# Kernel tuning notes

Measured on AMD Instinct MI355X. Metric: run time of the kernel, lower is better.

## Reference

```python
import jax, jax.numpy as jnp
import numpy as np

A_DIM = 6
VBR = jnp.array([300.0, 750.0, 1200.0, 1850.0, 2850.0, 4300.0])
MAX_BR = 4300.0
BUF = 30000.0  # buffer_size fixed to 30000 each forward
N_STEPS = 6    # unrolled iterations in the source (cooked_bw[0]..cooked_bw[5])


def _conv_feat(x, w, b):
    # 1-channel valid Conv1d(kernel=4) + ReLU, flattened channel-major like torch .view
    L = x.shape[0]
    idx = jnp.arange(L - 3)[:, None] + jnp.arange(4)[None, :]
    win = x[idx]                                   # (L-3, 4)
    out = jax.nn.relu(win @ w[:, 0, :].T + b)      # (L-3, 128)
    return out.T.reshape(-1)                       # (128*(L-3),)


def setup_inputs() -> dict:
    key = jax.random.key(0)
    ks = jax.random.split(key, 12)
    s = 0.1
    return {
        "inp": jax.random.uniform(ks[0], (8, 8), jnp.float32) + 0.1,
        "conv_w": jax.random.normal(ks[1], (128, 1, 4), jnp.float32) * s,
        "conv_b": jax.random.normal(ks[2], (128,), jnp.float32) * s,
        "w0": jax.random.normal(ks[3], (128, 1), jnp.float32) * s,
        "b0": jax.random.normal(ks[4], (128,), jnp.float32) * s,
        "w1": jax.random.normal(ks[5], (128, 1), jnp.float32) * s,
        "b1": jax.random.normal(ks[6], (128,), jnp.float32) * s,
        "w2": jax.random.normal(ks[7], (128, 1), jnp.float32) * s,
        "b2": jax.random.normal(ks[8], (128,), jnp.float32) * s,
        "w3": jax.random.normal(ks[9], (128, 2048), jnp.float32) * 0.02,
        "b3": jax.random.normal(ks[10], (128,), jnp.float32) * s,
        "w4": jax.random.normal(ks[11], (6, 128), jnp.float32) * s,
        "b4": jnp.zeros((6,), jnp.float32),
    }


def reference(inp, conv_w, conv_b, w0, b0, w1, b1, w2, b2, w3, b3, w4, b4):
    state = inp[:6, :]          # (6, 8)
    bw = inp[6, :]              # cooked bandwidth trace
    vs = inp[7, 0]              # base video chunk size
    vcs = vs * jnp.array([1.0, 2.0, 4.0, 8.0, 16.0, 32.0])  # video_chunk_sizes

    def net(st):
        s0 = jax.nn.relu(st[0, -1] * w0[:, 0] + b0)
        s1 = jax.nn.relu(st[1, -1] * w1[:, 0] + b1)
        s2 = _conv_feat(st[2, :], conv_w, conv_b)          # 640
        s3 = _conv_feat(st[3, :], conv_w, conv_b)          # 640
        s4 = _conv_feat(st[4, :A_DIM], conv_w, conv_b)     # 384
        s5 = st[4, -1] * w2[:, 0] + b2                     # no relu (matches source)
        feat = jnp.concatenate([s0, s1, s2, s3, s4, s5])   # (2048,)
        h = jax.nn.relu(w3 @ feat + b3)
        return w4 @ h + b4                                 # (6,)

    for i in range(N_STEPS):
        logits = net(state)
        a = jnp.argmax(logits)
        state = jnp.roll(state, -1, axis=1)
        delay = vcs[a] / bw[i] - BUF
        state = state.at[0, -1].set(VBR[a] / MAX_BR)
        state = state.at[1, -1].set(BUF / 1000.0 / 10.0)
        state = state.at[2, -1].set(vcs[a] / delay / 1000.0)
        state = state.at[3, -1].set(delay / 1000.0 / 10.0)
        state = state.at[4, :A_DIM].set(vcs / 1e6)
        state = state.at[5, -1].set((7.0 - i) / 8.0)

    return net(state)
```

## Files before the change

### kernel.cpp

```cpp
#include <hip/hip_runtime.h>

#define NBLK 32
#define TPB  256
#define FSTRIDE 32
#define PSTRIDE 64

__device__ __forceinline__ float relu_(float x) { return fmaxf(x, 0.f); }


__launch_bounds__(TPB, 1)
__global__ void actor_kernel(
    const float* __restrict__ inp,
    const float* __restrict__ conv_w, const float* __restrict__ conv_b,
    const float* __restrict__ w0, const float* __restrict__ b0,
    const float* __restrict__ w1, const float* __restrict__ b1,
    const float* __restrict__ w2, const float* __restrict__ b2,
    const float* __restrict__ w3, const float* __restrict__ b3,
    const float* __restrict__ w4, const float* __restrict__ b4,
    float* __restrict__ out, int* __restrict__ flags,
    float* __restrict__ partials)
{
    const int tid = threadIdx.x;
    const int b   = blockIdx.x;

    __shared__ __align__(16) float lw3[4 * 2048];
    __shared__ __align__(16) float lfeat[2048];
    __shared__ __align__(16) float lc2[512], lc3[512];
    __shared__ float lbase2[128], lbase3[128], ls5[128];
    __shared__ float ls0[6 * 128];
    __shared__ float ltmp[512];
    __shared__ __align__(16) float lcw[512];
    __shared__ float lcb[128];
    __shared__ float lw0v[128], lb0v[128], lw1v[128], lb1v[128];
    __shared__ float lw2v[128], lb2v[128], lb3v[128];
    __shared__ float lw4[768], lb4v[8];
    __shared__ float st2[8], st3[8], st4[8];
    __shared__ float sx[8];
    __shared__ float lbw[8];
    __shared__ float h_lds[4], hv_lds[4 * 8];
    __shared__ float red[48];

    {
        const float4* g4 = (const float4*)(w3 + b * 4 * 2048);
        float4* l4 = (float4*)lw3;
        for (int idx = tid; idx < 2048; idx += TPB) l4[idx] = g4[idx];
    }
    for (int idx = tid; idx < 512; idx += TPB) lcw[idx] = conv_w[idx];
    if (tid < 128) {
        lcb[tid]  = conv_b[tid];
        lw0v[tid] = w0[tid]; lb0v[tid] = b0[tid];
        lw1v[tid] = w1[tid]; lb1v[tid] = b1[tid];
        lw2v[tid] = w2[tid]; lb2v[tid] = b2[tid];
        lb3v[tid] = b3[tid];
    }
    for (int idx = tid; idx < 768; idx += TPB) lw4[idx] = w4[idx];
    if (tid < 6) lb4v[tid] = b4[tid];
    if (tid < 8) {
        st2[tid] = inp[16 + tid];
        st3[tid] = inp[24 + tid];
        st4[tid] = inp[32 + tid];
        lbw[tid] = inp[48 + tid];
    }
    if (tid == 0) {
        sx[0] = inp[7];   sx[1] = inp[15];
        sx[2] = inp[39];  sx[3] = inp[32];
        sx[4] = inp[56];
    }
    __syncthreads();

    if (tid < 128) {
        const float vb[6] = {300.f, 750.f, 1200.f, 1850.f, 2850.f, 4300.f};
        #pragma unroll
        for (int v = 0; v < 6; ++v)
            ls0[v * 128 + tid] = relu_(vb[v] * (1.f / 4300.f) * lw0v[tid] + lb0v[tid]);
        ltmp[tid] = relu_(3.0f * lw1v[tid] + lb1v[tid]);
    }
    for (int m = tid; m < 384; m += TPB) {
        int c = m / 3, w = m - c * 3;
        float a = lcb[c];
        #pragma unroll
        for (int k = 0; k < 4; ++k)
            a += sx[4] * (float)(1 << (w + k)) * 1e-6f * lcw[c * 4 + k];
        ltmp[128 + m] = relu_(a);
    }
    __syncthreads();

    const int wv = tid >> 6, lane = tid & 63;
    const float* wr = lw3 + wv * 2048;
    const float bias3 = lb3v[b * 4 + wv];

    float hs0p[6], hs14p;
    #pragma unroll
    for (int v = 0; v < 6; ++v)
        hs0p[v] = wr[lane] * ls0[v * 128 + lane] + wr[64 + lane] * ls0[v * 128 + 64 + lane];
    hs14p = wr[128 + lane] * ltmp[lane] + wr[192 + lane] * ltmp[64 + lane];
    #pragma unroll
    for (int k = 0; k < 6; ++k) {
        int m = lane + 64 * k;
        hs14p += wr[1536 + m] * ltmp[128 + m];
    }

    const float VBRc[6] = {300.f, 750.f, 1200.f, 1850.f, 2850.f, 4300.f};

    for (int g = 0; g < 3; ++g) {
        const int i = 2 * g;

        if (tid < 128) {
            lfeat[tid]        = relu_(sx[0] * lw0v[tid] + lb0v[tid]);
            lfeat[1920 + tid] =        sx[2] * lw2v[tid] + lb2v[tid];
            lbase2[tid] = st2[5] * lcw[tid*4] + st2[6] * lcw[tid*4+1]
                        + st2[7] * lcw[tid*4+2] + lcb[tid];
            lbase3[tid] = st3[5] * lcw[tid*4] + st3[6] * lcw[tid*4+1]
                        + st3[7] * lcw[tid*4+2] + lcb[tid];
            ls5[tid] = sx[3] * lw2v[tid] + lb2v[tid];
        } else {
            int j = tid - 128;
            lfeat[128 + j] = relu_(sx[1] * lw1v[j] + lb1v[j]);
        }
        for (int m = tid; m < 640; m += TPB) {
            int c = m / 5, w = m - c * 5;
            float a2 = lcb[c], a3 = lcb[c];
            #pragma unroll
            for (int k = 0; k < 4; ++k) {
                float cw = lcw[c * 4 + k];
                a2 += st2[w + k] * cw;
                a3 += st3[w + k] * cw;
            }
            lfeat[256 + m] = relu_(a2);
            lfeat[896 + m] = relu_(a3);
        }
        for (int m = tid; m < 384; m += TPB) {
            int c = m / 3, w = m - c * 3;
            float a4 = lcb[c];
            #pragma unroll
            for (int k = 0; k < 4; ++k) a4 += st4[w + k] * lcw[c * 4 + k];
            lfeat[1536 + m] = relu_(a4);
        }
        for (int m = tid; m < 512; m += TPB) {
            int c = m >> 2, w = m & 3;
            float a2 = lcb[c], a3 = lcb[c];
            #pragma unroll
            for (int k = 0; k < 4; ++k) {
                float cw = lcw[c * 4 + k];
                a2 += st2[w + 1 + k] * cw;
                a3 += st3[w + 1 + k] * cw;
            }
            lc2[m] = relu_(a2);
            lc3[m] = relu_(a3);
        }
        __syncthreads();

        float acc_i;
        {
            const float4* w4p = (const float4*)wr;
            const float4* f4p = (const float4*)lfeat;
            float4 acc = make_float4(0.f, 0.f, 0.f, 0.f);
            #pragma unroll
            for (int it = 0; it < 8; ++it) {
                float4 a = w4p[it * 64 + lane];
                float4 f = f4p[it * 64 + lane];
                acc.x += a.x * f.x; acc.y += a.y * f.y;
                acc.z += a.z * f.z; acc.w += a.w * f.w;
            }
            acc_i = (acc.x + acc.y) + (acc.z + acc.w);
        }

        float acc_c = hs14p
                    + wr[1920 + lane] * ls5[lane]
                    + wr[1984 + lane] * ls5[64 + lane];
        #pragma unroll
        for (int k = 0; k < 8; ++k) {
            int m = lane + 64 * k;
            int col = 256 + (m >> 2) * 5 + (m & 3);
            acc_c += wr[col] * lc2[m] + wr[640 + col] * lc3[m];
        }

        float n2[6], n3[6];
        {
            float bwi = lbw[i], vs = sx[4];
            #pragma unroll
            for (int v = 0; v < 6; ++v) {
                float vca   = vs * (float)(1 << v);
                float delay = vca / bwi - 30000.f;
                n2[v] = vca / delay * 1e-3f;
                n3[v] = delay * 1e-4f;
            }
        }
        float accv[6];
        #pragma unroll
        for (int v = 0; v < 6; ++v) accv[v] = hs0p[v];
        #pragma unroll
        for (int t = 0; t < 2; ++t) {
            int c = lane + 64 * t;
            float cw3 = lcw[c * 4 + 3];
            float bb2 = lbase2[c], bb3 = lbase3[c];
            float wc2 = wr[256 + c * 5 + 4], wc3 = wr[896 + c * 5 + 4];
            #pragma unroll
            for (int v = 0; v < 6; ++v)
                accv[v] += relu_(bb2 + n2[v] * cw3) * wc2
                         + relu_(bb3 + n3[v] * cw3) * wc3;
        }

        #pragma unroll
        for (int off = 32; off > 0; off >>= 1) {
            acc_i += __shfl_xor(acc_i, off);
            acc_c += __shfl_xor(acc_c, off);
            #pragma unroll
            for (int v = 0; v < 6; ++v) accv[v] += __shfl_xor(accv[v], off);
        }
        if (lane == 0) {
            h_lds[wv] = relu_(acc_i + bias3);
            #pragma unroll
            for (int v = 0; v < 6; ++v)
                hv_lds[wv * 8 + v] = relu_(acc_c + accv[v] + bias3);
        }
        __syncthreads();

        if (tid < 42) {
            int q = tid / 6, t = tid - q * 6;
            float p = 0.f;
            if (q == 0) {
                #pragma unroll
                for (int w = 0; w < 4; ++w) p += lw4[t * 128 + b * 4 + w] * h_lds[w];
            } else {
                #pragma unroll
                for (int w = 0; w < 4; ++w) p += lw4[t * 128 + b * 4 + w] * hv_lds[w * 8 + (q - 1)];
            }
            __hip_atomic_store(&partials[(g * NBLK + b) * PSTRIDE + tid], p,
                               __ATOMIC_RELAXED, __HIP_MEMORY_SCOPE_AGENT);
        }
        __syncthreads();
        if (tid == 0)
            __hip_atomic_store(&flags[b * FSTRIDE], g + 1,
                               __ATOMIC_RELEASE, __HIP_MEMORY_SCOPE_AGENT);
        if (tid < NBLK) {
            while (__hip_atomic_load(&flags[tid * FSTRIDE], __ATOMIC_ACQUIRE,
                                     __HIP_MEMORY_SCOPE_AGENT) < g + 1)
                __builtin_amdgcn_s_sleep(1);
        }
        __syncthreads();

        if (tid < 42) {
            float p = lb4v[tid % 6];
            #pragma unroll
            for (int bb = 0; bb < NBLK; ++bb)
                p += __hip_atomic_load(&partials[(g * NBLK + bb) * PSTRIDE + tid],
                                       __ATOMIC_RELAXED, __HIP_MEMORY_SCOPE_AGENT);
            red[tid] = p;
        }
        __syncthreads();
        if (tid == 0) {
            float best = red[0]; int a0 = 0;
            #pragma unroll
            for (int r = 1; r < 6; ++r) if (red[r] > best) { best = red[r]; a0 = r; }
            best = red[6 + 6 * a0]; int a1 = 0;
            #pragma unroll
            for (int r = 1; r < 6; ++r)
                if (red[6 + 6 * a0 + r] > best) { best = red[6 + 6 * a0 + r]; a1 = r; }

            {
                float vca = sx[4] * (float)(1 << a0);
                float delay = vca / lbw[i] - 30000.f;
                sx[0] = VBRc[a0] * (1.f / 4300.f);
                sx[1] = 3.0f;
                #pragma unroll
                for (int c = 0; c < 7; ++c) { st2[c] = st2[c + 1]; st3[c] = st3[c + 1]; }
                st2[7] = vca / delay * 1e-3f;
                st3[7] = delay * 1e-4f;
                sx[2] = sx[3]; sx[3] = sx[4] * 1e-6f;
                #pragma unroll
                for (int j = 0; j < 6; ++j) st4[j] = sx[4] * (float)(1 << j) * 1e-6f;
            }
            {
                float vca = sx[4] * (float)(1 << a1);
                float delay = vca / lbw[i + 1] - 30000.f;
                sx[0] = VBRc[a1] * (1.f / 4300.f);
                sx[1] = 3.0f;
                #pragma unroll
                for (int c = 0; c < 7; ++c) { st2[c] = st2[c + 1]; st3[c] = st3[c + 1]; }
                st2[7] = vca / delay * 1e-3f;
                st3[7] = delay * 1e-4f;
                sx[2] = sx[3]; sx[3] = sx[4] * 1e-6f;
                #pragma unroll
                for (int j = 0; j < 6; ++j) st4[j] = sx[4] * (float)(1 << j) * 1e-6f;
            }
        }
        __syncthreads();
    }

    if (tid < 128) {
        lfeat[tid]        = relu_(sx[0] * lw0v[tid] + lb0v[tid]);
        lfeat[1920 + tid] =        sx[2] * lw2v[tid] + lb2v[tid];
    } else {
        int j = tid - 128;
        lfeat[128 + j] = relu_(sx[1] * lw1v[j] + lb1v[j]);
    }
    for (int m = tid; m < 640; m += TPB) {
        int c = m / 5, w = m - c * 5;
        float a2 = lcb[c], a3 = lcb[c];
        #pragma unroll
        for (int k = 0; k < 4; ++k) {
            float cw = lcw[c * 4 + k];
            a2 += st2[w + k] * cw;
            a3 += st3[w + k] * cw;
        }
        lfeat[256 + m] = relu_(a2);
        lfeat[896 + m] = relu_(a3);
    }
    for (int m = tid; m < 384; m += TPB) {
        int c = m / 3, w = m - c * 3;
        float a4 = lcb[c];
        #pragma unroll
        for (int k = 0; k < 4; ++k) a4 += st4[w + k] * lcw[c * 4 + k];
        lfeat[1536 + m] = relu_(a4);
    }
    __syncthreads();
    {
        const float4* w4p = (const float4*)wr;
        const float4* f4p = (const float4*)lfeat;
        float4 acc = make_float4(0.f, 0.f, 0.f, 0.f);
        #pragma unroll
        for (int it = 0; it < 8; ++it) {
            float4 a = w4p[it * 64 + lane];
            float4 f = f4p[it * 64 + lane];
            acc.x += a.x * f.x; acc.y += a.y * f.y;
            acc.z += a.z * f.z; acc.w += a.w * f.w;
        }
        float s = (acc.x + acc.y) + (acc.z + acc.w);
        #pragma unroll
        for (int off = 32; off > 0; off >>= 1) s += __shfl_xor(s, off);
        if (lane == 0) h_lds[wv] = relu_(s + bias3);
    }
    __syncthreads();
    if (tid < 6) {
        float p = 0.f;
        #pragma unroll
        for (int w = 0; w < 4; ++w) p += lw4[tid * 128 + b * 4 + w] * h_lds[w];
        __hip_atomic_store(&partials[(3 * NBLK + b) * PSTRIDE + tid], p,
                           __ATOMIC_RELAXED, __HIP_MEMORY_SCOPE_AGENT);
    }
    __syncthreads();
    if (tid == 0)
        __hip_atomic_store(&flags[b * FSTRIDE], 4,
                           __ATOMIC_RELEASE, __HIP_MEMORY_SCOPE_AGENT);
    if (b == 0) {
        if (tid < NBLK) {
            while (__hip_atomic_load(&flags[tid * FSTRIDE], __ATOMIC_ACQUIRE,
                                     __HIP_MEMORY_SCOPE_AGENT) < 4)
                __builtin_amdgcn_s_sleep(1);
        }
        __syncthreads();
        if (tid < 6) {
            float p = lb4v[tid];
            #pragma unroll
            for (int bb = 0; bb < NBLK; ++bb)
                p += __hip_atomic_load(&partials[(3 * NBLK + bb) * PSTRIDE + tid],
                                       __ATOMIC_RELAXED, __HIP_MEMORY_SCOPE_AGENT);
            out[tid] = p;
        }
    }
}

extern "C" void kernel_launch(void* const* d_in, const int* in_sizes, int n_in,
                              void* d_out, int out_size, void* d_ws, size_t ws_size,
                              hipStream_t stream) {
    const float* inp    = (const float*)d_in[0];
    const float* conv_w = (const float*)d_in[1];
    const float* conv_b = (const float*)d_in[2];
    const float* w0     = (const float*)d_in[3];
    const float* b0     = (const float*)d_in[4];
    const float* w1     = (const float*)d_in[5];
    const float* b1     = (const float*)d_in[6];
    const float* w2     = (const float*)d_in[7];
    const float* b2     = (const float*)d_in[8];
    const float* w3     = (const float*)d_in[9];
    const float* b3     = (const float*)d_in[10];
    const float* w4     = (const float*)d_in[11];
    const float* b4     = (const float*)d_in[12];

    int*   flags    = (int*)d_ws;
    float* partials = (float*)((char*)d_ws + 8192);

    actor_kernel<<<NBLK, TPB, 0, stream>>>(inp, conv_w, conv_b,
                                           w0, b0, w1, b1, w2, b2,
                                           w3, b3, w4, b4,
                                           (float*)d_out, flags, partials);
}
```

Measured before the change: 99.95 us.

## Pack partials with epoch tags into 64-bit words to drop flag barrier

Each block now publishes every partial logit as a 64-bit word holding the float value and the step tag. This replaces the separate partial store plus release flag and block barrier. Readers poll the tagged words directly, with the gather split across 168 threads and then reduced in shared memory. The goal is to remove the extra syncthreads, the flag round-trip and the serial 32-way load per thread on the inter-block exchange path. In exchange it polls many more addresses, and any stale tags left in the workspace from earlier launches could match early.

```diff
diff --git a/kernel.cpp b/kernel.cpp
--- a/kernel.cpp
+++ b/kernel.cpp
@@ -2,8 +2,6 @@
 
 #define NBLK 32
 #define TPB  256
-#define FSTRIDE 32
-#define PSTRIDE 64
 
 __device__ __forceinline__ float relu_(float x) { return fmaxf(x, 0.f); }
 
@@ -17,8 +15,7 @@
     const float* __restrict__ w2, const float* __restrict__ b2,
     const float* __restrict__ w3, const float* __restrict__ b3,
     const float* __restrict__ w4, const float* __restrict__ b4,
-    float* __restrict__ out, int* __restrict__ flags,
-    float* __restrict__ partials)
+    float* __restrict__ out, unsigned long long* __restrict__ pub)
 {
     const int tid = threadIdx.x;
     const int b   = blockIdx.x;
@@ -38,6 +35,7 @@
     __shared__ float sx[8];
     __shared__ float lbw[8];
     __shared__ float h_lds[4], hv_lds[4 * 8];
+    __shared__ float s_red[192];
     __shared__ float red[48];
 
     {
@@ -226,29 +224,46 @@
                 #pragma unroll
                 for (int w = 0; w < 4; ++w) p += lw4[t * 128 + b * 4 + w] * hv_lds[w * 8 + (q - 1)];
             }
-            __hip_atomic_store(&partials[(g * NBLK + b) * PSTRIDE + tid], p,
+            unsigned long long val =
+                ((unsigned long long)__float_as_uint(p) << 32) | (unsigned)(g + 1);
+            __hip_atomic_store(&pub[(g * NBLK + b) * 64 + tid], val,
                                __ATOMIC_RELAXED, __HIP_MEMORY_SCOPE_AGENT);
         }
-        __syncthreads();
-        if (tid == 0)
-            __hip_atomic_store(&flags[b * FSTRIDE], g + 1,
-                               __ATOMIC_RELEASE, __HIP_MEMORY_SCOPE_AGENT);
-        if (tid < NBLK) {
-            while (__hip_atomic_load(&flags[tid * FSTRIDE], __ATOMIC_ACQUIRE,
-                                     __HIP_MEMORY_SCOPE_AGENT) < g + 1)
+
+        if (tid < 168) {
+            int j = tid >> 2, part = tid & 3;
+            const unsigned long long* base = &pub[(g * NBLK + part * 8) * 64 + j];
+            unsigned long long v[8];
+            #pragma unroll
+            for (int k = 0; k < 8; ++k)
+                v[k] = __hip_atomic_load(base + k * 64, __ATOMIC_ACQUIRE,
+                                         __HIP_MEMORY_SCOPE_AGENT);
+            for (;;) {
+                bool all = true;
+                #pragma unroll
+                for (int k = 0; k < 8; ++k)
+                    all = all && ((unsigned)v[k] == (unsigned)(g + 1));
+                if (all) break;
                 __builtin_amdgcn_s_sleep(1);
-        }
-        __syncthreads();
-
-        if (tid < 42) {
-            float p = lb4v[tid % 6];
-            #pragma unroll
-            for (int bb = 0; bb < NBLK; ++bb)
-                p += __hip_atomic_load(&partials[(g * NBLK + bb) * PSTRIDE + tid],
-                                       __ATOMIC_RELAXED, __HIP_MEMORY_SCOPE_AGENT);
-            red[tid] = p;
-        }
-        __syncthreads();
+                #pragma unroll
+                for (int k = 0; k < 8; ++k)
+                    if ((unsigned)v[k] != (unsigned)(g + 1))
+                        v[k] = __hip_atomic_load(base + k * 64, __ATOMIC_ACQUIRE,
+                                                 __HIP_MEMORY_SCOPE_AGENT);
+            }
+            float p = 0.f;
+            #pragma unroll
+            for (int k = 0; k < 8; ++k)
+                p += __uint_as_float((unsigned)(v[k] >> 32));
+            s_red[j * 4 + part] = p;
+        }
+        __syncthreads();
+        if (tid < 42)
+            red[tid] = lb4v[tid % 6]
+                     + ((s_red[tid * 4] + s_red[tid * 4 + 1])
+                      + (s_red[tid * 4 + 2] + s_red[tid * 4 + 3]));
+        __syncthreads();
+
         if (tid == 0) {
             float best = red[0]; int a0 = 0;
             #pragma unroll
@@ -336,26 +351,29 @@
         float p = 0.f;
         #pragma unroll
         for (int w = 0; w < 4; ++w) p += lw4[tid * 128 + b * 4 + w] * h_lds[w];
-        __hip_atomic_store(&partials[(3 * NBLK + b) * PSTRIDE + tid], p,
+        unsigned long long val =
+            ((unsigned long long)__float_as_uint(p) << 32) | 4u;
+        __hip_atomic_store(&pub[(3 * NBLK + b) * 64 + tid], val,
                            __ATOMIC_RELAXED, __HIP_MEMORY_SCOPE_AGENT);
     }
-    __syncthreads();
-    if (tid == 0)
-        __hip_atomic_store(&flags[b * FSTRIDE], 4,
-                           __ATOMIC_RELEASE, __HIP_MEMORY_SCOPE_AGENT);
     if (b == 0) {
-        if (tid < NBLK) {
-            while (__hip_atomic_load(&flags[tid * FSTRIDE], __ATOMIC_ACQUIRE,
-                                     __HIP_MEMORY_SCOPE_AGENT) < 4)
+        if (tid < 192) {
+            int j = tid >> 5, bb = tid & 31;
+            unsigned long long v =
+                __hip_atomic_load(&pub[(3 * NBLK + bb) * 64 + j],
+                                  __ATOMIC_ACQUIRE, __HIP_MEMORY_SCOPE_AGENT);
+            while ((unsigned)v != 4u) {
                 __builtin_amdgcn_s_sleep(1);
+                v = __hip_atomic_load(&pub[(3 * NBLK + bb) * 64 + j],
+                                      __ATOMIC_ACQUIRE, __HIP_MEMORY_SCOPE_AGENT);
+            }
+            s_red[j * 32 + bb] = __uint_as_float((unsigned)(v >> 32));
         }
         __syncthreads();
         if (tid < 6) {
             float p = lb4v[tid];
             #pragma unroll
-            for (int bb = 0; bb < NBLK; ++bb)
-                p += __hip_atomic_load(&partials[(3 * NBLK + bb) * PSTRIDE + tid],
-                                       __ATOMIC_RELAXED, __HIP_MEMORY_SCOPE_AGENT);
+            for (int bb = 0; bb < NBLK; ++bb) p += s_red[tid * 32 + bb];
             out[tid] = p;
         }
     }
@@ -378,11 +396,10 @@
     const float* w4     = (const float*)d_in[11];
     const float* b4     = (const float*)d_in[12];
 
-    int*   flags    = (int*)d_ws;
-    float* partials = (float*)((char*)d_ws + 8192);
+    unsigned long long* pub = (unsigned long long*)d_ws;
 
     actor_kernel<<<NBLK, TPB, 0, stream>>>(inp, conv_w, conv_b,
                                            w0, b0, w1, b1, w2, b2,
                                            w3, b3, w4, b4,
-                                           (float*)d_out, flags, partials);
+                                           (float*)d_out, pub);
 }
```

New measurement: 113.7 us. +13.7%, slower.

## Speculatively evaluate final two steps for all 36 action pairs to cut a grid barrier

Applied to the files above, without the earlier changes.

Replaces the last loop iteration and the final network pass with one phase. For step 4, each block computes logits for all six step-5 candidates and for all 36 (a4, a5) action pairs of the final pass. Block 0 reduces the 258 partials, picks the actions by argmax and outputs the matching logits. This removes one cross-block flag round-trip, but adds much more per-thread work and register use (42 extra accumulators) and a larger partials buffer.

```diff
diff --git a/kernel.cpp b/kernel.cpp
--- a/kernel.cpp
+++ b/kernel.cpp
@@ -3,7 +3,7 @@
 #define NBLK 32
 #define TPB  256
 #define FSTRIDE 32
-#define PSTRIDE 64
+#define PSTRIDE 320
 
 __device__ __forceinline__ float relu_(float x) { return fmaxf(x, 0.f); }
 
@@ -38,7 +38,10 @@
     __shared__ float sx[8];
     __shared__ float lbw[8];
     __shared__ float h_lds[4], hv_lds[4 * 8];
+    __shared__ float hf_lds[4 * 40];
     __shared__ float red[48];
+    __shared__ float red2[264];
+    __shared__ int   ssel;
 
     {
         const float4* g4 = (const float4*)(w3 + b * 4 * 2048);
@@ -102,7 +105,7 @@
 
     const float VBRc[6] = {300.f, 750.f, 1200.f, 1850.f, 2850.f, 4300.f};
 
-    for (int g = 0; g < 3; ++g) {
+    for (int g = 0; g < 2; ++g) {
         const int i = 2 * g;
 
         if (tid < 128) {
@@ -288,75 +291,212 @@
         __syncthreads();
     }
 
-    if (tid < 128) {
-        lfeat[tid]        = relu_(sx[0] * lw0v[tid] + lb0v[tid]);
-        lfeat[1920 + tid] =        sx[2] * lw2v[tid] + lb2v[tid];
-    } else {
-        int j = tid - 128;
-        lfeat[128 + j] = relu_(sx[1] * lw1v[j] + lb1v[j]);
-    }
-    for (int m = tid; m < 640; m += TPB) {
-        int c = m / 5, w = m - c * 5;
-        float a2 = lcb[c], a3 = lcb[c];
-        #pragma unroll
-        for (int k = 0; k < 4; ++k) {
-            float cw = lcw[c * 4 + k];
-            a2 += st2[w + k] * cw;
-            a3 += st3[w + k] * cw;
-        }
-        lfeat[256 + m] = relu_(a2);
-        lfeat[896 + m] = relu_(a3);
-    }
-    for (int m = tid; m < 384; m += TPB) {
-        int c = m / 3, w = m - c * 3;
-        float a4 = lcb[c];
-        #pragma unroll
-        for (int k = 0; k < 4; ++k) a4 += st4[w + k] * lcw[c * 4 + k];
-        lfeat[1536 + m] = relu_(a4);
-    }
-    __syncthreads();
     {
-        const float4* w4p = (const float4*)wr;
-        const float4* f4p = (const float4*)lfeat;
-        float4 acc = make_float4(0.f, 0.f, 0.f, 0.f);
-        #pragma unroll
-        for (int it = 0; it < 8; ++it) {
-            float4 a = w4p[it * 64 + lane];
-            float4 f = f4p[it * 64 + lane];
-            acc.x += a.x * f.x; acc.y += a.y * f.y;
-            acc.z += a.z * f.z; acc.w += a.w * f.w;
-        }
-        float s = (acc.x + acc.y) + (acc.z + acc.w);
-        #pragma unroll
-        for (int off = 32; off > 0; off >>= 1) s += __shfl_xor(s, off);
-        if (lane == 0) h_lds[wv] = relu_(s + bias3);
-    }
-    __syncthreads();
-    if (tid < 6) {
-        float p = 0.f;
-        #pragma unroll
-        for (int w = 0; w < 4; ++w) p += lw4[tid * 128 + b * 4 + w] * h_lds[w];
-        __hip_atomic_store(&partials[(3 * NBLK + b) * PSTRIDE + tid], p,
-                           __ATOMIC_RELAXED, __HIP_MEMORY_SCOPE_AGENT);
-    }
-    __syncthreads();
-    if (tid == 0)
-        __hip_atomic_store(&flags[b * FSTRIDE], 4,
-                           __ATOMIC_RELEASE, __HIP_MEMORY_SCOPE_AGENT);
-    if (b == 0) {
-        if (tid < NBLK) {
-            while (__hip_atomic_load(&flags[tid * FSTRIDE], __ATOMIC_ACQUIRE,
-                                     __HIP_MEMORY_SCOPE_AGENT) < 4)
-                __builtin_amdgcn_s_sleep(1);
-        }
-        __syncthreads();
-        if (tid < 6) {
-            float p = lb4v[tid];
-            #pragma unroll
-            for (int bb = 0; bb < NBLK; ++bb)
-                p += __hip_atomic_load(&partials[(3 * NBLK + bb) * PSTRIDE + tid],
-                                       __ATOMIC_RELAXED, __HIP_MEMORY_SCOPE_AGENT);
-            out[tid] = p;
+        const int i = 4;
+
+        if (tid < 128) {
+            lfeat[tid]        = relu_(sx[0] * lw0v[tid] + lb0v[tid]);
+            lfeat[1920 + tid] =        sx[2] * lw2v[tid] + lb2v[tid];
+            lbase2[tid] = st2[5] * lcw[tid*4] + st2[6] * lcw[tid*4+1]
+                        + st2[7] * lcw[tid*4+2] + lcb[tid];
+            lbase3[tid] = st3[5] * lcw[tid*4] + st3[6] * lcw[tid*4+1]
+                        + st3[7] * lcw[tid*4+2] + lcb[tid];
+            ls5[tid] = sx[3] * lw2v[tid] + lb2v[tid];
+        } else {
+            int j = tid - 128;
+            lfeat[128 + j] = relu_(sx[1] * lw1v[j] + lb1v[j]);
+        }
+        for (int m = tid; m < 640; m += TPB) {
+            int c = m / 5, w = m - c * 5;
+            float a2 = lcb[c], a3 = lcb[c];
+            #pragma unroll
+            for (int k = 0; k < 4; ++k) {
+                float cw = lcw[c * 4 + k];
+                a2 += st2[w + k] * cw;
+                a3 += st3[w + k] * cw;
+            }
+            lfeat[256 + m] = relu_(a2);
+            lfeat[896 + m] = relu_(a3);
+        }
+        for (int m = tid; m < 384; m += TPB) {
+            int c = m / 3, w = m - c * 3;
+            float a4 = lcb[c];
+            #pragma unroll
+            for (int k = 0; k < 4; ++k) a4 += st4[w + k] * lcw[c * 4 + k];
+            lfeat[1536 + m] = relu_(a4);
+        }
+        for (int m = tid; m < 512; m += TPB) {
+            int c = m >> 2, w = m & 3;
+            float a2 = lcb[c], a3 = lcb[c];
+            #pragma unroll
+            for (int k = 0; k < 4; ++k) {
+                float cw = lcw[c * 4 + k];
+                a2 += st2[w + 1 + k] * cw;
+                a3 += st3[w + 1 + k] * cw;
+            }
+            lc2[m] = relu_(a2);
+            lc3[m] = relu_(a3);
+        }
+        __syncthreads();
+
+        float acc_i;
+        {
+            const float4* w4p = (const float4*)wr;
+            const float4* f4p = (const float4*)lfeat;
+            float4 acc = make_float4(0.f, 0.f, 0.f, 0.f);
+            #pragma unroll
+            for (int it = 0; it < 8; ++it) {
+                float4 a = w4p[it * 64 + lane];
+                float4 f = f4p[it * 64 + lane];
+                acc.x += a.x * f.x; acc.y += a.y * f.y;
+                acc.z += a.z * f.z; acc.w += a.w * f.w;
+            }
+            acc_i = (acc.x + acc.y) + (acc.z + acc.w);
+        }
+
+        float s5c = wr[1920 + lane] * ls5[lane] + wr[1984 + lane] * ls5[64 + lane];
+        float acc_c = hs14p + s5c;
+        #pragma unroll
+        for (int k = 0; k < 8; ++k) {
+            int m = lane + 64 * k;
+            int col = 256 + (m >> 2) * 5 + (m & 3);
+            acc_c += wr[col] * lc2[m] + wr[640 + col] * lc3[m];
+        }
+
+        float n24[6], n34[6], n25[6], n35[6];
+        {
+            float bw4 = lbw[4], bw5 = lbw[5], vs = sx[4];
+            #pragma unroll
+            for (int v = 0; v < 6; ++v) {
+                float vca = vs * (float)(1 << v);
+                float d4  = vca / bw4 - 30000.f;
+                float d5  = vca / bw5 - 30000.f;
+                n24[v] = vca / d4 * 1e-3f;  n34[v] = d4 * 1e-4f;
+                n25[v] = vca / d5 * 1e-3f;  n35[v] = d5 * 1e-4f;
+            }
+        }
+
+        float cw0a[2], cw1a[2], cw2a[2], cw3a[2], lb2a[2], lb3a[2];
+        float wc2a[2], wc3a[2], w3s2[2], w3s3[2], b42a[2], b43a[2];
+        float fcom = hs14p + s5c;
+        #pragma unroll
+        for (int t = 0; t < 2; ++t) {
+            int c = lane + 64 * t;
+            cw0a[t] = lcw[c*4];   cw1a[t] = lcw[c*4+1];
+            cw2a[t] = lcw[c*4+2]; cw3a[t] = lcw[c*4+3];
+            lb2a[t] = lbase2[c];  lb3a[t] = lbase3[c];
+            wc2a[t] = wr[256 + c*5 + 4]; wc3a[t] = wr[896 + c*5 + 4];
+            w3s2[t] = wr[256 + c*5 + 3]; w3s3[t] = wr[896 + c*5 + 3];
+            b42a[t] = st2[6]*cw0a[t] + st2[7]*cw1a[t] + lcb[c];
+            b43a[t] = st3[6]*cw0a[t] + st3[7]*cw1a[t] + lcb[c];
+            #pragma unroll
+            for (int w = 0; w < 3; ++w) {
+                float a2 = st2[2+w]*cw0a[t] + st2[3+w]*cw1a[t]
+                         + st2[4+w]*cw2a[t] + st2[5+w]*cw3a[t] + lcb[c];
+                float a3 = st3[2+w]*cw0a[t] + st3[3+w]*cw1a[t]
+                         + st3[4+w]*cw2a[t] + st3[5+w]*cw3a[t] + lcb[c];
+                fcom += relu_(a2) * wr[256 + c*5 + w] + relu_(a3) * wr[896 + c*5 + w];
+            }
+        }
+
+        float accv[6], accf[36];
+        #pragma unroll
+        for (int v4 = 0; v4 < 6; ++v4) {
+            float av = hs0p[v4];
+            float fv4 = fcom;
+            #pragma unroll
+            for (int t = 0; t < 2; ++t) {
+                float r2 = relu_(lb2a[t] + n24[v4] * cw3a[t]);
+                float r3 = relu_(lb3a[t] + n34[v4] * cw3a[t]);
+                av  += r2 * wc2a[t] + r3 * wc3a[t];
+                fv4 += r2 * w3s2[t] + r3 * w3s3[t];
+            }
+            accv[v4] = av;
+            #pragma unroll
+            for (int v5 = 0; v5 < 6; ++v5) {
+                float s = fv4 + hs0p[v5];
+                #pragma unroll
+                for (int t = 0; t < 2; ++t) {
+                    s += relu_(b42a[t] + n24[v4]*cw2a[t] + n25[v5]*cw3a[t]) * wc2a[t]
+                       + relu_(b43a[t] + n34[v4]*cw2a[t] + n35[v5]*cw3a[t]) * wc3a[t];
+                }
+                accf[v4 * 6 + v5] = s;
+            }
+        }
+
+        #pragma unroll
+        for (int off = 32; off > 0; off >>= 1) {
+            acc_i += __shfl_xor(acc_i, off);
+            acc_c += __shfl_xor(acc_c, off);
+            #pragma unroll
+            for (int v = 0; v < 6; ++v) accv[v] += __shfl_xor(accv[v], off);
+            #pragma unroll
+            for (int v = 0; v < 36; ++v) accf[v] += __shfl_xor(accf[v], off);
+        }
+        if (lane == 0) {
+            h_lds[wv] = relu_(acc_i + bias3);
+            #pragma unroll
+            for (int v = 0; v < 6; ++v)
+                hv_lds[wv * 8 + v] = relu_(acc_c + accv[v] + bias3);
+            #pragma unroll
+            for (int v = 0; v < 36; ++v)
+                hf_lds[wv * 40 + v] = relu_(accf[v] + bias3);
+        }
+        __syncthreads();
+
+        float* slot = &partials[(2 * NBLK + b) * PSTRIDE];
+        if (tid < 42) {
+            int q = tid / 6, t = tid - q * 6;
+            float p = 0.f;
+            if (q == 0) {
+                #pragma unroll
+                for (int w = 0; w < 4; ++w) p += lw4[t * 128 + b * 4 + w] * h_lds[w];
+            } else {
+                #pragma unroll
+                for (int w = 0; w < 4; ++w) p += lw4[t * 128 + b * 4 + w] * hv_lds[w * 8 + (q - 1)];
+            }
+            __hip_atomic_store(&slot[tid], p, __ATOMIC_RELAXED, __HIP_MEMORY_SCOPE_AGENT);
+        }
+        if (tid < 216) {
+            int combo = tid / 6, t = tid - combo * 6;
+            float p = 0.f;
+            #pragma unroll
+            for (int w = 0; w < 4; ++w) p += lw4[t * 128 + b * 4 + w] * hf_lds[w * 40 + combo];
+            __hip_atomic_store(&slot[42 + tid], p, __ATOMIC_RELAXED, __HIP_MEMORY_SCOPE_AGENT);
+        }
+        __syncthreads();
+        if (tid == 0)
+            __hip_atomic_store(&flags[b * FSTRIDE], 3,
+                               __ATOMIC_RELEASE, __HIP_MEMORY_SCOPE_AGENT);
+
+        if (b == 0) {
+            if (tid < NBLK) {
+                while (__hip_atomic_load(&flags[tid * FSTRIDE], __ATOMIC_ACQUIRE,
+                                         __HIP_MEMORY_SCOPE_AGENT) < 3)
+                    __builtin_amdgcn_s_sleep(1);
+            }
+            __syncthreads();
+            for (int v = tid; v < 258; v += TPB) {
+                float p = lb4v[v % 6];
+                #pragma unroll
+                for (int bb = 0; bb < NBLK; ++bb)
+                    p += __hip_atomic_load(&partials[(2 * NBLK + bb) * PSTRIDE + v],
+                                           __ATOMIC_RELAXED, __HIP_MEMORY_SCOPE_AGENT);
+                red2[v] = p;
+            }
+            __syncthreads();
+            if (tid == 0) {
+                float best = red2[0]; int a4 = 0;
+                #pragma unroll
+                for (int r = 1; r < 6; ++r) if (red2[r] > best) { best = red2[r]; a4 = r; }
+                best = red2[6 + 6 * a4]; int a5 = 0;
+                #pragma unroll
+                for (int r = 1; r < 6; ++r)
+                    if (red2[6 + 6 * a4 + r] > best) { best = red2[6 + 6 * a4 + r]; a5 = r; }
+                ssel = a4 * 6 + a5;
+            }
+            __syncthreads();
+            if (tid < 6) out[tid] = red2[42 + ssel * 6 + tid];
         }
     }
 }
```

New measurement: 102.2 us. +2.3%, slower.

## Precompute final-step features in registers and skip last state update pass

Applied to the files above, without the earlier changes.

During the last group, each lane precomputes the parts of the final network evaluation that do not depend on the last two chosen actions, keeping them in registers. The final forward pass then reduces to a few relu terms selected by the chosen actions, replacing the full feature rebuild, a barrier and the full 2048-wide dot product. Block 0's final reduction also loads the partials in parallel across threads into shared memory instead of issuing serial atomic loads from six threads. This adds register pressure and depends on the incremental decomposition staying exact for the rolled state.

```diff
diff --git a/kernel.cpp b/kernel.cpp
--- a/kernel.cpp
+++ b/kernel.cpp
@@ -39,6 +39,8 @@
     __shared__ float lbw[8];
     __shared__ float h_lds[4], hv_lds[4 * 8];
     __shared__ float red[48];
+    __shared__ float s_red[192];
+    __shared__ int   sact[2];
 
     {
         const float4* g4 = (const float4*)(w3 + b * 4 * 2048);
@@ -101,6 +103,10 @@
     }
 
     const float VBRc[6] = {300.f, 750.f, 1200.f, 1850.f, 2850.f, 4300.f};
+
+    float fcom_f = 0.f;
+    float lb2s[2], lb3s[2], b4f2[2], b4f3[2];
+    float cw2s[2], cw3s[2], w32s[2], w33s[2], w42s[2], w43s[2];
 
     for (int g = 0; g < 3; ++g) {
         const int i = 2 * g;
@@ -165,9 +171,8 @@
             acc_i = (acc.x + acc.y) + (acc.z + acc.w);
         }
 
-        float acc_c = hs14p
-                    + wr[1920 + lane] * ls5[lane]
-                    + wr[1984 + lane] * ls5[64 + lane];
+        float s5c = wr[1920 + lane] * ls5[lane] + wr[1984 + lane] * ls5[64 + lane];
+        float acc_c = hs14p + s5c;
         #pragma unroll
         for (int k = 0; k < 8; ++k) {
             int m = lane + 64 * k;
@@ -199,6 +204,27 @@
             for (int v = 0; v < 6; ++v)
                 accv[v] += relu_(bb2 + n2[v] * cw3) * wc2
                          + relu_(bb3 + n3[v] * cw3) * wc3;
+        }
+
+        if (g == 2) {
+            fcom_f = hs14p + s5c;
+            #pragma unroll
+            for (int t = 0; t < 2; ++t) {
+                int c = lane + 64 * t;
+                float c0 = lcw[c*4], c1 = lcw[c*4+1], c2 = lcw[c*4+2], c3 = lcw[c*4+3];
+                cw2s[t] = c2; cw3s[t] = c3;
+                lb2s[t] = lbase2[c];  lb3s[t] = lbase3[c];
+                b4f2[t] = st2[6]*c0 + st2[7]*c1 + lcb[c];
+                b4f3[t] = st3[6]*c0 + st3[7]*c1 + lcb[c];
+                w32s[t] = wr[256 + c*5 + 3]; w33s[t] = wr[896 + c*5 + 3];
+                w42s[t] = wr[256 + c*5 + 4]; w43s[t] = wr[896 + c*5 + 4];
+                #pragma unroll
+                for (int w = 0; w < 3; ++w) {
+                    float a2 = st2[2+w]*c0 + st2[3+w]*c1 + st2[4+w]*c2 + st2[5+w]*c3 + lcb[c];
+                    float a3 = st3[2+w]*c0 + st3[3+w]*c1 + st3[4+w]*c2 + st3[5+w]*c3 + lcb[c];
+                    fcom_f += relu_(a2) * wr[256 + c*5 + w] + relu_(a3) * wr[896 + c*5 + w];
+                }
+            }
         }
 
         #pragma unroll
@@ -258,78 +284,69 @@
             for (int r = 1; r < 6; ++r)
                 if (red[6 + 6 * a0 + r] > best) { best = red[6 + 6 * a0 + r]; a1 = r; }
 
-            {
-                float vca = sx[4] * (float)(1 << a0);
-                float delay = vca / lbw[i] - 30000.f;
-                sx[0] = VBRc[a0] * (1.f / 4300.f);
-                sx[1] = 3.0f;
-                #pragma unroll
-                for (int c = 0; c < 7; ++c) { st2[c] = st2[c + 1]; st3[c] = st3[c + 1]; }
-                st2[7] = vca / delay * 1e-3f;
-                st3[7] = delay * 1e-4f;
-                sx[2] = sx[3]; sx[3] = sx[4] * 1e-6f;
-                #pragma unroll
-                for (int j = 0; j < 6; ++j) st4[j] = sx[4] * (float)(1 << j) * 1e-6f;
-            }
-            {
-                float vca = sx[4] * (float)(1 << a1);
-                float delay = vca / lbw[i + 1] - 30000.f;
-                sx[0] = VBRc[a1] * (1.f / 4300.f);
-                sx[1] = 3.0f;
-                #pragma unroll
-                for (int c = 0; c < 7; ++c) { st2[c] = st2[c + 1]; st3[c] = st3[c + 1]; }
-                st2[7] = vca / delay * 1e-3f;
-                st3[7] = delay * 1e-4f;
-                sx[2] = sx[3]; sx[3] = sx[4] * 1e-6f;
-                #pragma unroll
-                for (int j = 0; j < 6; ++j) st4[j] = sx[4] * (float)(1 << j) * 1e-6f;
-            }
-        }
-        __syncthreads();
-    }
-
-    if (tid < 128) {
-        lfeat[tid]        = relu_(sx[0] * lw0v[tid] + lb0v[tid]);
-        lfeat[1920 + tid] =        sx[2] * lw2v[tid] + lb2v[tid];
-    } else {
-        int j = tid - 128;
-        lfeat[128 + j] = relu_(sx[1] * lw1v[j] + lb1v[j]);
-    }
-    for (int m = tid; m < 640; m += TPB) {
-        int c = m / 5, w = m - c * 5;
-        float a2 = lcb[c], a3 = lcb[c];
-        #pragma unroll
-        for (int k = 0; k < 4; ++k) {
-            float cw = lcw[c * 4 + k];
-            a2 += st2[w + k] * cw;
-            a3 += st3[w + k] * cw;
-        }
-        lfeat[256 + m] = relu_(a2);
-        lfeat[896 + m] = relu_(a3);
-    }
-    for (int m = tid; m < 384; m += TPB) {
-        int c = m / 3, w = m - c * 3;
-        float a4 = lcb[c];
-        #pragma unroll
-        for (int k = 0; k < 4; ++k) a4 += st4[w + k] * lcw[c * 4 + k];
-        lfeat[1536 + m] = relu_(a4);
-    }
-    __syncthreads();
+            if (g == 2) {
+                sact[0] = a0; sact[1] = a1;
+            } else {
+                {
+                    float vca = sx[4] * (float)(1 << a0);
+                    float delay = vca / lbw[i] - 30000.f;
+                    sx[0] = VBRc[a0] * (1.f / 4300.f);
+                    sx[1] = 3.0f;
+                    #pragma unroll
+                    for (int c = 0; c < 7; ++c) { st2[c] = st2[c + 1]; st3[c] = st3[c + 1]; }
+                    st2[7] = vca / delay * 1e-3f;
+                    st3[7] = delay * 1e-4f;
+                    sx[2] = sx[3]; sx[3] = sx[4] * 1e-6f;
+                    #pragma unroll
+                    for (int j = 0; j < 6; ++j) st4[j] = sx[4] * (float)(1 << j) * 1e-6f;
+                }
+                {
+                    float vca = sx[4] * (float)(1 << a1);
+                    float delay = vca / lbw[i + 1] - 30000.f;
+                    sx[0] = VBRc[a1] * (1.f / 4300.f);
+                    sx[1] = 3.0f;
+                    #pragma unroll
+                    for (int c = 0; c < 7; ++c) { st2[c] = st2[c + 1]; st3[c] = st3[c + 1]; }
+                    st2[7] = vca / delay * 1e-3f;
+                    st3[7] = delay * 1e-4f;
+                    sx[2] = sx[3]; sx[3] = sx[4] * 1e-6f;
+                    #pragma unroll
+                    for (int j = 0; j < 6; ++j) st4[j] = sx[4] * (float)(1 << j) * 1e-6f;
+                }
+            }
+        }
+        __syncthreads();
+    }
+
     {
-        const float4* w4p = (const float4*)wr;
-        const float4* f4p = (const float4*)lfeat;
-        float4 acc = make_float4(0.f, 0.f, 0.f, 0.f);
-        #pragma unroll
-        for (int it = 0; it < 8; ++it) {
-            float4 a = w4p[it * 64 + lane];
-            float4 f = f4p[it * 64 + lane];
-            acc.x += a.x * f.x; acc.y += a.y * f.y;
-            acc.z += a.z * f.z; acc.w += a.w * f.w;
-        }
-        float s = (acc.x + acc.y) + (acc.z + acc.w);
-        #pragma unroll
-        for (int off = 32; off > 0; off >>= 1) s += __shfl_xor(s, off);
-        if (lane == 0) h_lds[wv] = relu_(s + bias3);
+        const int a4 = sact[0], a5 = sact[1];
+        float vs = sx[4];
+        float vca4 = vs * (float)(1 << a4);
+        float d4   = vca4 / lbw[4] - 30000.f;
+        float ap24 = vca4 / d4 * 1e-3f, ap34 = d4 * 1e-4f;
+        float vca5 = vs * (float)(1 << a5);
+        float d5   = vca5 / lbw[5] - 30000.f;
+        float ap25 = vca5 / d5 * 1e-3f, ap35 = d5 * 1e-4f;
+
+        float h0 = hs0p[0];
+        h0 = (a5 == 1) ? hs0p[1] : h0;
+        h0 = (a5 == 2) ? hs0p[2] : h0;
+        h0 = (a5 == 3) ? hs0p[3] : h0;
+        h0 = (a5 == 4) ? hs0p[4] : h0;
+        h0 = (a5 == 5) ? hs0p[5] : h0;
+
+        float hl = fcom_f + h0;
+        #pragma unroll
+        for (int t = 0; t < 2; ++t) {
+            float r32 = relu_(lb2s[t] + ap24 * cw3s[t]);
+            float r33 = relu_(lb3s[t] + ap34 * cw3s[t]);
+            float r42 = relu_(b4f2[t] + ap24 * cw2s[t] + ap25 * cw3s[t]);
+            float r43 = relu_(b4f3[t] + ap34 * cw2s[t] + ap35 * cw3s[t]);
+            hl += r32 * w32s[t] + r33 * w33s[t] + r42 * w42s[t] + r43 * w43s[t];
+        }
+        #pragma unroll
+        for (int off = 32; off > 0; off >>= 1) hl += __shfl_xor(hl, off);
+        if (lane == 0) h_lds[wv] = relu_(hl + bias3);
     }
     __syncthreads();
     if (tid < 6) {
@@ -350,12 +367,17 @@
                 __builtin_amdgcn_s_sleep(1);
         }
         __syncthreads();
+        if (tid < 192) {
+            int j = tid >> 5, bb = tid & 31;
+            s_red[j * 32 + bb] =
+                __hip_atomic_load(&partials[(3 * NBLK + bb) * PSTRIDE + j],
+                                  __ATOMIC_RELAXED, __HIP_MEMORY_SCOPE_AGENT);
+        }
+        __syncthreads();
         if (tid < 6) {
             float p = lb4v[tid];
             #pragma unroll
-            for (int bb = 0; bb < NBLK; ++bb)
-                p += __hip_atomic_load(&partials[(3 * NBLK + bb) * PSTRIDE + tid],
-                                       __ATOMIC_RELAXED, __HIP_MEMORY_SCOPE_AGENT);
+            for (int bb = 0; bb < NBLK; ++bb) p += s_red[tid * 32 + bb];
             out[tid] = p;
         }
     }
```

After: 99.84 us. Within noise of the previous version (-0.1%).
